# Performance work log

Measured on AMD Instinct MI355X. Metric: run time of the kernel, lower is better.

Reference implementation:

```python
import jax, jax.numpy as jnp
import numpy as np

B, S, D = 4, 2048, 1024
NH = 16
H2 = NH // 2
F = D // NH  # per-head hidden = 64
EXP = 4
DECAY_CONST = S // 512  # 4
EPS = 1e-5


def setup_inputs() -> dict:
    key = jax.random.key(0)
    ks = jax.random.split(key, 8)
    inp = {
        "x": jax.random.normal(ks[0], (B, S, D), dtype=jnp.float32),
        # token_norm / channel_norm params (LayerNorm init: ones/zeros)
        "g1": jnp.ones((D,), jnp.float32), "b1": jnp.zeros((D,), jnp.float32),
        "g2": jnp.ones((D,), jnp.float32), "b2": jnp.zeros((D,), jnp.float32),
        # per-head input projections [NH, D, F] and output projection
        "Wp": jax.random.normal(ks[1], (NH, D, F), jnp.float32) * 0.02,
        "bp": jnp.zeros((NH, F), jnp.float32),
        "Wo": jax.random.normal(ks[2], (D, D), jnp.float32) * 0.02,
        "bo": jnp.zeros((D,), jnp.float32),
        # ColRepeatCausalLinear: weight = 0.4, bias = 3 ; RowRepeat: -0.3, 0.2
        "w_col": jnp.full((H2, S), 0.4, jnp.float32),
        "b_col": jnp.full((H2, S), 3.0, jnp.float32),
        "w_row": jnp.full((H2, S), -0.3, jnp.float32),
        "b_row": jnp.full((H2, S), 0.2, jnp.float32),
        # decay_value params (ones, clipped to [0.9, 1] then ** (1/decay_constant))
        "dcol": jnp.ones((H2,), jnp.float32),
        "drow": jnp.ones((H2,), jnp.float32),
        # channel MLP
        "W1": jax.random.normal(ks[3], (D, EXP * D), jnp.float32) * 0.02,
        "c1": jnp.zeros((EXP * D,), jnp.float32),
        "W2": jax.random.normal(ks[4], (EXP * D, D), jnp.float32) * 0.02,
        "c2": jnp.zeros((D,), jnp.float32),
    }
    return inp


def _ln(x, g, b):
    m = jnp.mean(x, axis=-1, keepdims=True)
    v = jnp.mean(jnp.square(x - m), axis=-1, keepdims=True)
    return (x - m) * jax.lax.rsqrt(v + EPS) * g + b


def _forward(x, g1, b1, g2, b2, Wp, bp, Wo, bo, w_col, b_col, w_row, b_row,
             dcol, drow, W1, c1, W2, c2):
    decay_c = jnp.clip(dcol, 0.9, 1.0) ** (1.0 / DECAY_CONST)  # [H2]
    decay_r = jnp.clip(drow, 0.9, 1.0) ** (1.0 / DECAY_CONST)  # [H2]

    def step(carry, inp):
        cc, rc = carry                      # each [B, H2, F]
        xt, wc, bc, wr, br = inp            # xt [B, D]; wc/bc/wr/br [H2]
        # token mixing branch
        h = _ln(xt, g1, b1)
        proj = jnp.einsum('bd,hdf->bhf', h, Wp) + bp  # [B, NH, F]
        # Col heads: cache = proj + decay*cache ; out = w*cache + b
        cc = proj[:, :H2] + decay_c[None, :, None] * cc
        col_out = wc[None, :, None] * cc + bc[None, :, None]
        # Row heads: cache = w*proj + decay*cache ; out = cache + b
        rc = wr[None, :, None] * proj[:, H2:] + decay_r[None, :, None] * rc
        row_out = rc + br[None, :, None]
        mix = jnp.concatenate([col_out, row_out], axis=1).reshape(xt.shape[0], -1)
        y = xt + mix @ Wo + bo
        # channel MLP branch
        h2 = _ln(y, g2, b2)
        out = y + jax.nn.gelu(h2 @ W1 + c1) @ W2 + c2
        return (cc, rc), out

    init = (jnp.zeros((x.shape[0], H2, F), x.dtype),
            jnp.zeros((x.shape[0], H2, F), x.dtype))
    xs = (jnp.swapaxes(x, 0, 1), w_col.T, b_col.T, w_row.T, b_row.T)
    _, ys = jax.lax.scan(step, init, xs)    # ys [S, B, D]
    return jnp.swapaxes(ys, 0, 1)


def reference(x, g1, b1, g2, b2, Wp, bp, Wo, bo, w_col, b_col, w_row, b_row,
              dcol, drow, W1, c1, W2, c2):
    return _forward(x, g1, b1, g2, b2, Wp, bp, Wo, bo, w_col, b_col,
                    w_row, b_row, dcol, drow, W1, c1, W2, c2)
```

## Files before the change

### kernel.cpp

```cpp
#include <hip/hip_runtime.h>

typedef __attribute__((ext_vector_type(4))) float fx4;
typedef __attribute__((ext_vector_type(8))) short s16x8;
typedef __attribute__((ext_vector_type(2))) unsigned long long u64x2;

#define SEQ   2048
#define DM    1024
#define BSZ   4
#define ROWS  (BSZ*SEQ)
#define CHUNK 64
#define NCH   (SEQ/CHUNK)

__device__ __forceinline__ unsigned short f2bf(float f){
  unsigned u = __builtin_bit_cast(unsigned, f);
  u = u + 0x7FFFu + ((u >> 16) & 1u);
  return (unsigned short)(u >> 16);
}
__device__ __forceinline__ float bf2f(unsigned short u){
  return __builtin_bit_cast(float, ((unsigned)u) << 16);
}

__device__ __forceinline__ unsigned char f2fp8(float x){
  unsigned u = __builtin_bit_cast(unsigned, x);
  unsigned s = (u >> 24) & 0x80u;
  float ax = __builtin_fabsf(x);
  if (ax >= 448.f) return (unsigned char)(s | 0x7Eu);
  if (ax < 0.015625f){
    int m = (int)(ax * 512.f + 0.5f);
    return (unsigned char)(s | (unsigned)m);
  }
  unsigned b = __builtin_bit_cast(unsigned, ax);
  b += 0x0007FFFFu + ((b >> 20) & 1u);
  unsigned e = (b >> 23) - 127u + 7u;
  unsigned m = (b >> 20) & 7u;
  return (unsigned char)(s | (e << 3) | m);
}

__device__ __forceinline__ float gelu_f(float x){
  float u = 0.7978845608028654f * (x + 0.044715f * x*x*x);
  return x / (1.0f + __expf(-2.0f*u));
}

__device__ __forceinline__ void gload_lds16(const void* g, void* l){
  __builtin_amdgcn_global_load_lds(
      (__attribute__((address_space(1))) void*)g,
      (__attribute__((address_space(3))) void*)l, 16, 0, 0);
}

__device__ __forceinline__ fx4 mfma_fp8(unsigned long long a, unsigned long long b, fx4 c){
  return __builtin_amdgcn_mfma_f32_16x16x32_fp8_fp8((long)a, (long)b, c, 0, 0, 0);
}

__global__ __launch_bounds__(256) void transpose_k(const float* __restrict__ in,
    unsigned short* __restrict__ out, int R, int C, long long ibs, long long obs){
  __shared__ float tile[32][33];
  in  += (long long)blockIdx.z * ibs;
  out += (long long)blockIdx.z * obs;
  int c0 = blockIdx.x*32, r0 = blockIdx.y*32;
  int tx = threadIdx.x, ty = threadIdx.y;
  #pragma unroll
  for (int i=0;i<4;i++)
    tile[ty+8*i][tx] = in[(long long)(r0+ty+8*i)*C + c0+tx];
  __syncthreads();
  #pragma unroll
  for (int i=0;i<4;i++)
    out[(long long)(c0+ty+8*i)*R + r0+tx] = f2bf(tile[tx][ty+8*i]);
}

__global__ __launch_bounds__(256) void transpose_f8(const float* __restrict__ in,
    unsigned char* __restrict__ out, int R, int C){
  __shared__ float tile[32][33];
  int c0 = blockIdx.x*32, r0 = blockIdx.y*32;
  int tx = threadIdx.x, ty = threadIdx.y;
  #pragma unroll
  for (int i=0;i<4;i++)
    tile[ty+8*i][tx] = in[(long long)(r0+ty+8*i)*C + c0+tx];
  __syncthreads();
  #pragma unroll
  for (int i=0;i<4;i++)
    out[(long long)(c0+ty+8*i)*R + r0+tx] = f2fp8(tile[tx][ty+8*i] * 64.f);
}

__global__ __launch_bounds__(256) void ln_rows(const float* __restrict__ x,
    const float* __restrict__ g, const float* __restrict__ b,
    unsigned short* __restrict__ out){
  int row = blockIdx.x, t = threadIdx.x;
  const fx4* xr = (const fx4*)(x + (long long)row*DM);
  fx4 v = xr[t];
  float s  = v[0]+v[1]+v[2]+v[3];
  float s2 = v[0]*v[0]+v[1]*v[1]+v[2]*v[2]+v[3]*v[3];
  #pragma unroll
  for (int o=32;o;o>>=1){ s += __shfl_down(s,o); s2 += __shfl_down(s2,o); }
  __shared__ float red[8];
  int lane = t & 63, wid = t >> 6;
  if (lane==0){ red[wid]=s; red[4+wid]=s2; }
  __syncthreads();
  s  = red[0]+red[1]+red[2]+red[3];
  s2 = red[4]+red[5]+red[6]+red[7];
  float m  = s * (1.0f/DM);
  float rs = rsqrtf(s2*(1.0f/DM) - m*m + 1e-5f);
  const fx4 gv = ((const fx4*)g)[t], bv = ((const fx4*)b)[t];
  ushort4 pk;
  pk.x = f2bf((v[0]-m)*rs*gv[0] + bv[0]);
  pk.y = f2bf((v[1]-m)*rs*gv[1] + bv[1]);
  pk.z = f2bf((v[2]-m)*rs*gv[2] + bv[2]);
  pk.w = f2bf((v[3]-m)*rs*gv[3] + bv[3]);
  *(ushort4*)(out + (long long)row*DM + t*4) = pk;
}

__global__ __launch_bounds__(256) void ln_rows_f8(const float* __restrict__ x,
    const float* __restrict__ g, const float* __restrict__ b,
    unsigned char* __restrict__ out){
  int row = blockIdx.x, t = threadIdx.x;
  const fx4* xr = (const fx4*)(x + (long long)row*DM);
  fx4 v = xr[t];
  float s  = v[0]+v[1]+v[2]+v[3];
  float s2 = v[0]*v[0]+v[1]*v[1]+v[2]*v[2]+v[3]*v[3];
  #pragma unroll
  for (int o=32;o;o>>=1){ s += __shfl_down(s,o); s2 += __shfl_down(s2,o); }
  __shared__ float red[8];
  int lane = t & 63, wid = t >> 6;
  if (lane==0){ red[wid]=s; red[4+wid]=s2; }
  __syncthreads();
  s  = red[0]+red[1]+red[2]+red[3];
  s2 = red[4]+red[5]+red[6]+red[7];
  float m  = s * (1.0f/DM);
  float rs = rsqrtf(s2*(1.0f/DM) - m*m + 1e-5f);
  const fx4 gv = ((const fx4*)g)[t], bv = ((const fx4*)b)[t];
  uchar4 pk;
  pk.x = f2fp8((v[0]-m)*rs*gv[0] + bv[0]);
  pk.y = f2fp8((v[1]-m)*rs*gv[1] + bv[1]);
  pk.z = f2fp8((v[2]-m)*rs*gv[2] + bv[2]);
  pk.w = f2fp8((v[3]-m)*rs*gv[3] + bv[3]);
  *(uchar4*)(out + (long long)row*DM + t*4) = pk;
}

__global__ __launch_bounds__(256) void scan_carry(const unsigned short* __restrict__ P,
    const float* __restrict__ w_row, const float* __restrict__ dcol,
    const float* __restrict__ drow, float* __restrict__ carry){
  int g = blockIdx.x*4 + (threadIdx.x>>6);
  int lane = threadIdx.x & 63;
  int chunk = g & (NCH-1); int bh = g >> 5; int h = bh & 15; int b = bh >> 4;
  float draw = (h<8) ? dcol[h] : drow[h-8];
  float d = powf(fminf(fmaxf(draw,0.9f),1.0f), 0.25f);
  float c = 0.f;
  const unsigned short* p = P + ((long long)(b*SEQ + chunk*CHUNK))*DM + h*64 + lane;
  const float* wr = w_row + (h>=8 ? (h-8)*SEQ + chunk*CHUNK : 0);
  #pragma unroll 4
  for (int i=0;i<CHUNK;i++){
    float a = bf2f(p[(long long)i*DM]);
    if (h>=8) a *= wr[i];
    c = fmaf(d, c, a);
  }
  carry[((long long)(bh*64 + lane))*NCH + chunk] = c;
}

__global__ __launch_bounds__(256) void scan_final(const unsigned short* __restrict__ P,
    const float* __restrict__ w_col, const float* __restrict__ b_col,
    const float* __restrict__ w_row, const float* __restrict__ b_row,
    const float* __restrict__ dcol, const float* __restrict__ drow,
    const float* __restrict__ carry, unsigned short* __restrict__ mix){
  int g = blockIdx.x*4 + (threadIdx.x>>6);
  int lane = threadIdx.x & 63;
  int chunk = g & (NCH-1); int bh = g >> 5; int h = bh & 15; int b = bh >> 4;
  float draw = (h<8) ? dcol[h] : drow[h-8];
  float d = powf(fminf(fmaxf(draw,0.9f),1.0f), 0.25f);
  float dL = d;
  #pragma unroll
  for (int i=0;i<6;i++) dL *= dL;
  const float* cr = carry + ((long long)(bh*64 + lane))*NCH;
  float c = 0.f;
  for (int j=0;j<chunk;j++) c = fmaf(dL, c, cr[j]);
  const unsigned short* p = P + ((long long)(b*SEQ + chunk*CHUNK))*DM + h*64 + lane;
  unsigned short* mo = mix + ((long long)(b*SEQ + chunk*CHUNK))*DM + h*64 + lane;
  int t0 = chunk*CHUNK;
  #pragma unroll 4
  for (int i=0;i<CHUNK;i++){
    int t = t0 + i;
    float a = bf2f(p[(long long)i*DM]);
    float o;
    if (h<8){
      c = fmaf(d, c, a);
      o = w_col[h*SEQ + t]*c + b_col[h*SEQ + t];
    } else {
      a *= w_row[(h-8)*SEQ + t];
      c = fmaf(d, c, a);
      o = c + b_row[(h-8)*SEQ + t];
    }
    mo[(long long)i*DM] = f2bf(o);
  }
}

template<int EPI, int K>
__global__ __launch_bounds__(256) void gemm_bt(const unsigned short* __restrict__ A,
    const unsigned short* __restrict__ Bt, int N,
    const float* __restrict__ bias, const float* __restrict__ res,
    float* __restrict__ outf, unsigned short* __restrict__ outb){
  __shared__ __align__(16) unsigned short lds[16384];
  const int tid = threadIdx.x;
  const int l = tid & 63;
  const int w = tid >> 6;
  const int wr = w >> 1, wc = w & 1;
  const long long row0 = (long long)blockIdx.x * 128;
  const long long col0 = (long long)blockIdx.y * 128;

  fx4 acc[4][4] = {};

  const unsigned short* gA[4];
  const unsigned short* gB[4];
  int lslot[4];
  #pragma unroll
  for (int i=0;i<4;i++){
    int slot = w*256 + i*64 + l;
    int r = slot >> 3;
    int qs = slot & 7;
    int c = (qs ^ (r & 7)) << 3;
    gA[i] = A  + (row0 + r)*(long long)K + c;
    gB[i] = Bt + (col0 + r)*(long long)K + c;
    lslot[i] = slot*8;
  }
  int aoff[2][4], boff[2][4];
  #pragma unroll
  for (int kk=0;kk<2;kk++){
    #pragma unroll
    for (int m=0;m<4;m++){
      int r  = wr*64 + m*16 + (l&15);
      int q  = (kk*4 + (l>>4)) ^ (r&7);
      aoff[kk][m] = r*64 + q*8;
      int r2 = wc*64 + m*16 + (l&15);
      int q2 = (kk*4 + (l>>4)) ^ (r2&7);
      boff[kk][m] = 8192 + r2*64 + q2*8;
    }
  }

  const int nsteps = K >> 6;
  for (int s = 0; s < nsteps; ++s){
    #pragma unroll
    for (int i=0;i<4;i++){
      gload_lds16(gA[i], &lds[lslot[i]]);
      gload_lds16(gB[i], &lds[8192 + lslot[i]]);
      gA[i] += 64; gB[i] += 64;
    }
    __syncthreads();
    #pragma unroll
    for (int kk=0;kk<2;kk++){
      s16x8 af[4], bfr[4];
      #pragma unroll
      for (int m=0;m<4;m++) af[m]  = *(const s16x8*)&lds[aoff[kk][m]];
      #pragma unroll
      for (int n=0;n<4;n++) bfr[n] = *(const s16x8*)&lds[boff[kk][n]];
      #pragma unroll
      for (int m=0;m<4;m++)
        #pragma unroll
        for (int n=0;n<4;n++)
          acc[m][n] = __builtin_amdgcn_mfma_f32_16x16x32_bf16(af[m], bfr[n], acc[m][n], 0, 0, 0);
    }
    __syncthreads();
  }

  float* lf = (float*)lds;
  const int lg = l >> 4, lc = l & 15;
  #pragma unroll
  for (int g=0; g<4; ++g){
    if (wr == (g>>1)){
      #pragma unroll
      for (int mm=0; mm<2; ++mm){
        const int m = (g&1)*2 + mm;
        int lrow = mm*16 + lg*4;
        #pragma unroll
        for (int n=0;n<4;n++){
          int col = wc*64 + n*16 + lc;
          #pragma unroll
          for (int rg=0;rg<4;rg++)
            lf[(lrow+rg)*132 + col] = acc[m][n][rg];
        }
      }
    }
    __syncthreads();
    #pragma unroll
    for (int j=0;j<4;j++){
      int flat = j*256 + tid;
      int lrow = flat >> 5, c4 = flat & 31;
      long long grow = row0 + g*32 + lrow;
      long long gcol = col0 + c4*4;
      fx4 v = *(fx4*)&lf[lrow*132 + c4*4];
      fx4 bv = *(const fx4*)&bias[gcol];
      v = v + bv;
      long long idx = grow*(long long)N + gcol;
      if constexpr (EPI==1){
        fx4 rv = *(const fx4*)&res[idx];
        v = v + rv;
        *(fx4*)&outf[idx] = v;
      } else {
        ushort4 pk;
        pk.x = f2bf(v[0]); pk.y = f2bf(v[1]);
        pk.z = f2bf(v[2]); pk.w = f2bf(v[3]);
        *(ushort4*)&outb[idx] = pk;
      }
    }
    __syncthreads();
  }
}

template<int EPI, int K>
__global__ __launch_bounds__(256) void gemm_f8(const unsigned char* __restrict__ A,
    const unsigned char* __restrict__ Bt, int N,
    const float* __restrict__ bias, const float* __restrict__ res,
    float* __restrict__ outf, unsigned char* __restrict__ outb){
  __shared__ __align__(16) unsigned char lds[17408];
  const int tid = threadIdx.x;
  const int l = tid & 63;
  const int w = tid >> 6;
  const int wr = w >> 1, wc = w & 1;
  const long long row0 = (long long)blockIdx.x * 128;
  const long long col0 = (long long)blockIdx.y * 128;

  fx4 acc[4][4] = {};

  const unsigned char* gA[2];
  const unsigned char* gB[2];
  int lslot[2];
  #pragma unroll
  for (int i=0;i<2;i++){
    int slot = w*128 + i*64 + l;
    int r = slot >> 2;
    int q = slot & 3;
    int c = (q ^ (r & 3)) << 4;
    gA[i] = A  + (row0 + r)*(long long)K + c;
    gB[i] = Bt + (col0 + r)*(long long)K + c;
    lslot[i] = slot*16;
  }
  const int lg = l >> 4, l15 = l & 15;
  int aoff[4], boff[4];
  #pragma unroll
  for (int m=0;m<4;m++){
    int r  = wr*64 + m*16 + l15;
    aoff[m] = r*64 + ((lg ^ (r&3)) << 4);
    int r2 = wc*64 + m*16 + l15;
    boff[m] = 8192 + r2*64 + ((lg ^ (r2&3)) << 4);
  }

  const int nsteps = K >> 6;
  for (int s = 0; s < nsteps; ++s){
    #pragma unroll
    for (int i=0;i<2;i++){
      gload_lds16(gA[i], &lds[lslot[i]]);
      gload_lds16(gB[i], &lds[8192 + lslot[i]]);
      gA[i] += 64; gB[i] += 64;
    }
    __syncthreads();
    u64x2 a2[4], b2[4];
    #pragma unroll
    for (int m=0;m<4;m++) a2[m] = *(const u64x2*)&lds[aoff[m]];
    #pragma unroll
    for (int n=0;n<4;n++) b2[n] = *(const u64x2*)&lds[boff[n]];
    #pragma unroll
    for (int m=0;m<4;m++)
      #pragma unroll
      for (int n=0;n<4;n++)
        acc[m][n] = mfma_fp8(a2[m][0], b2[n][0], acc[m][n]);
    #pragma unroll
    for (int m=0;m<4;m++)
      #pragma unroll
      for (int n=0;n<4;n++)
        acc[m][n] = mfma_fp8(a2[m][1], b2[n][1], acc[m][n]);
    __syncthreads();
  }

  float* lf = (float*)lds;
  #pragma unroll
  for (int g=0; g<4; ++g){
    if (wr == (g>>1)){
      #pragma unroll
      for (int mm=0; mm<2; ++mm){
        const int m = (g&1)*2 + mm;
        int lrow = mm*16 + lg*4;
        #pragma unroll
        for (int n=0;n<4;n++){
          int col = wc*64 + n*16 + l15;
          #pragma unroll
          for (int rg=0;rg<4;rg++)
            lf[(lrow+rg)*132 + col] = acc[m][n][rg];
        }
      }
    }
    __syncthreads();
    #pragma unroll
    for (int j=0;j<4;j++){
      int flat = j*256 + tid;
      int lrow = flat >> 5, c4 = flat & 31;
      long long grow = row0 + g*32 + lrow;
      long long gcol = col0 + c4*4;
      fx4 v = *(fx4*)&lf[lrow*132 + c4*4];
      fx4 bv2 = *(const fx4*)&bias[gcol];
      v = v * 0.015625f + bv2;
      long long idx = grow*(long long)N + gcol;
      if constexpr (EPI==1){
        fx4 rv = *(const fx4*)&res[idx];
        v = v + rv;
        *(fx4*)&outf[idx] = v;
      } else {
        uchar4 pk;
        pk.x = f2fp8(gelu_f(v[0]));
        pk.y = f2fp8(gelu_f(v[1]));
        pk.z = f2fp8(gelu_f(v[2]));
        pk.w = f2fp8(gelu_f(v[3]));
        *(uchar4*)&outb[idx] = pk;
      }
    }
    __syncthreads();
  }
}

extern "C" void kernel_launch(void* const* d_in, const int* in_sizes, int n_in,
                              void* d_out, int out_size, void* d_ws, size_t ws_size,
                              hipStream_t stream){
  const float* x    = (const float*)d_in[0];
  const float* g1   = (const float*)d_in[1];
  const float* b1   = (const float*)d_in[2];
  const float* g2   = (const float*)d_in[3];
  const float* b2   = (const float*)d_in[4];
  const float* Wp   = (const float*)d_in[5];
  const float* bp   = (const float*)d_in[6];
  const float* Wo   = (const float*)d_in[7];
  const float* bo   = (const float*)d_in[8];
  const float* w_col= (const float*)d_in[9];
  const float* b_col= (const float*)d_in[10];
  const float* w_row= (const float*)d_in[11];
  const float* b_row= (const float*)d_in[12];
  const float* dcol = (const float*)d_in[13];
  const float* drow = (const float*)d_in[14];
  const float* W1   = (const float*)d_in[15];
  const float* c1   = (const float*)d_in[16];
  const float* W2   = (const float*)d_in[17];
  const float* c2   = (const float*)d_in[18];
  float* out = (float*)d_out;

  char* ws = (char*)d_ws;
  const size_t MB = 1024*1024;
  if (ws_size < 101*MB) return;
  unsigned short* Wpt  = (unsigned short*)(ws + 0);
  unsigned short* Wot  = (unsigned short*)(ws + 2*MB);
  unsigned char*  W1t8 = (unsigned char*)(ws + 4*MB);
  unsigned char*  W2t8 = (unsigned char*)(ws + 12*MB);
  unsigned short* h    = (unsigned short*)(ws + 20*MB);
  unsigned char*  yln8 = (unsigned char*)(ws + 20*MB);
  unsigned short* P    = (unsigned short*)(ws + 36*MB);
  unsigned char*  U8   = (unsigned char*)(ws + 36*MB);
  unsigned short* mix  = (unsigned short*)(ws + 68*MB);
  float*          carry= (float*)(ws + 84*MB);

  dim3 tb(32,8);
  transpose_k <<<dim3(2,32,16),  tb, 0, stream>>>(Wp, Wpt, 1024,   64, 65536LL, 65536LL);
  transpose_k <<<dim3(32,32,1),  tb, 0, stream>>>(Wo, Wot, 1024, 1024, 0LL, 0LL);
  transpose_f8<<<dim3(128,32,1), tb, 0, stream>>>(W1, W1t8, 1024, 4096);
  transpose_f8<<<dim3(32,128,1), tb, 0, stream>>>(W2, W2t8, 4096, 1024);

  ln_rows<<<dim3(ROWS), dim3(256), 0, stream>>>(x, g1, b1, h);
  gemm_bt<3,1024><<<dim3(64,8),  dim3(256), 0, stream>>>(h,   Wpt, 1024, bp, nullptr, nullptr, P);
  scan_carry<<<dim3(512), dim3(256), 0, stream>>>(P, w_row, dcol, drow, carry);
  scan_final<<<dim3(512), dim3(256), 0, stream>>>(P, w_col, b_col, w_row, b_row, dcol, drow, carry, mix);
  gemm_bt<1,1024><<<dim3(64,8),  dim3(256), 0, stream>>>(mix, Wot, 1024, bo, x, out, nullptr);
  ln_rows_f8<<<dim3(ROWS), dim3(256), 0, stream>>>(out, g2, b2, yln8);
  gemm_f8<2,1024><<<dim3(64,32), dim3(256), 0, stream>>>(yln8, W1t8, 4096, c1, nullptr, nullptr, U8);
  gemm_f8<1,4096><<<dim3(64,8),  dim3(256), 0, stream>>>(U8,  W2t8, 1024, c2, out, out, nullptr);
}
```

Before: 305.3 us.

## Triple-buffer LDS in FP8 GEMM with async prefetch two stages ahead

Restructures the FP8 GEMM main loop into a three-stage LDS ring buffer. Global-to-LDS loads are issued two K-steps ahead, and the loop waits with explicit vmcnt counts instead of two __syncthreads per step, so memory latency can overlap MFMA work. The XOR swizzle now uses (r>>1)&3 to change the LDS bank-conflict pattern. In exchange, LDS use per block rises to 48KB, which may lower occupancy, and the correctness of the single-barrier scheme depends on the vmcnt accounting.

```diff
diff --git a/kernel.cpp b/kernel.cpp
--- a/kernel.cpp
+++ b/kernel.cpp
@@ -307,7 +307,7 @@
     const unsigned char* __restrict__ Bt, int N,
     const float* __restrict__ bias, const float* __restrict__ res,
     float* __restrict__ outf, unsigned char* __restrict__ outb){
-  __shared__ __align__(16) unsigned char lds[17408];
+  __shared__ __align__(16) unsigned char lds[49152];
   const int tid = threadIdx.x;
   const int l = tid & 63;
   const int w = tid >> 6;
@@ -325,7 +325,7 @@
     int slot = w*128 + i*64 + l;
     int r = slot >> 2;
     int q = slot & 3;
-    int c = (q ^ (r & 3)) << 4;
+    int c = (q ^ ((r >> 1) & 3)) << 4;
     gA[i] = A  + (row0 + r)*(long long)K + c;
     gB[i] = Bt + (col0 + r)*(long long)K + c;
     lslot[i] = slot*16;
@@ -335,25 +335,39 @@
   #pragma unroll
   for (int m=0;m<4;m++){
     int r  = wr*64 + m*16 + l15;
-    aoff[m] = r*64 + ((lg ^ (r&3)) << 4);
+    aoff[m] = r*64 + ((lg ^ ((r >> 1) & 3)) << 4);
     int r2 = wc*64 + m*16 + l15;
-    boff[m] = 8192 + r2*64 + ((lg ^ (r2&3)) << 4);
-  }
+    boff[m] = 8192 + r2*64 + ((lg ^ ((r2 >> 1) & 3)) << 4);
+  }
+  auto STAGE = [&](int bufoff){
+    #pragma unroll
+    for (int i=0;i<2;i++){
+      gload_lds16(gA[i], &lds[bufoff + lslot[i]]);
+      gload_lds16(gB[i], &lds[bufoff + 8192 + lslot[i]]);
+      gA[i] += 64; gB[i] += 64;
+    }
+  };
 
   const int nsteps = K >> 6;
+  STAGE(0);
+  STAGE(16384);
+
+  int curoff = 0;
   for (int s = 0; s < nsteps; ++s){
-    #pragma unroll
-    for (int i=0;i<2;i++){
-      gload_lds16(gA[i], &lds[lslot[i]]);
-      gload_lds16(gB[i], &lds[8192 + lslot[i]]);
-      gA[i] += 64; gB[i] += 64;
-    }
-    __syncthreads();
+    if (s + 1 < nsteps) asm volatile("s_waitcnt vmcnt(4)" ::: "memory");
+    else                asm volatile("s_waitcnt vmcnt(0)" ::: "memory");
+    __builtin_amdgcn_sched_barrier(0);
+    __builtin_amdgcn_s_barrier();
+    __builtin_amdgcn_sched_barrier(0);
     u64x2 a2[4], b2[4];
     #pragma unroll
-    for (int m=0;m<4;m++) a2[m] = *(const u64x2*)&lds[aoff[m]];
-    #pragma unroll
-    for (int n=0;n<4;n++) b2[n] = *(const u64x2*)&lds[boff[n]];
+    for (int m=0;m<4;m++) a2[m] = *(const u64x2*)&lds[curoff + aoff[m]];
+    #pragma unroll
+    for (int n=0;n<4;n++) b2[n] = *(const u64x2*)&lds[curoff + boff[n]];
+    if (s + 2 < nsteps){
+      int nb = curoff + 32768; if (nb >= 49152) nb -= 49152;
+      STAGE(nb);
+    }
     #pragma unroll
     for (int m=0;m<4;m++)
       #pragma unroll
@@ -364,8 +378,9 @@
       #pragma unroll
       for (int n=0;n<4;n++)
         acc[m][n] = mfma_fp8(a2[m][1], b2[n][1], acc[m][n]);
-    __syncthreads();
-  }
+    curoff += 16384; if (curoff == 49152) curoff = 0;
+  }
+  __syncthreads();
 
   float* lf = (float*)lds;
   #pragma unroll
```

Measured after the change: 281.5 us. 1.08x faster.
